# Optimization experiments

Measured on AMD Instinct MI355X. Metric: run time of the kernel, lower is better.

## Reference

```python
import jax, jax.numpy as jnp
import numpy as np

D = 512      # d_model
H = 8        # n_head
NL = 3       # encoder layers
FF = 2048    # torch TransformerEncoderLayer default dim_feedforward
HID = 256    # hidden_size
ACT = 12     # action_size
NOBJ = 89    # num_objects
BAND = 17    # tril(diagonal=-17) -> keys older than 16 steps banned


def setup_inputs() -> dict:
    key = jax.random.key(0)
    ks = iter(jax.random.split(key, 48))
    rn = lambda shape, s=0.02: jax.random.normal(next(ks), shape, jnp.float32) * s
    b, seq = 16, 512
    inp = {
        'state_input': jax.random.normal(next(ks), (b, seq, 3, 16, 16), jnp.float32),
        'goal_input': jax.random.normal(next(ks), (b, seq, 300), jnp.float32),
        # encoders (stand-ins for obs_enc / lang_enc)
        'W_obs': rn((256, 3 * 16 * 16)), 'b_obs': rn((256,)),
        'W_lang': rn((256, 300)), 'b_lang': rn((256,)),
        # input projection 512 -> 512
        'W_in': rn((D, 512)), 'b_in': rn((D,)),
        # per-layer transformer params, stacked on layer dim
        'Wqkv': rn((NL, 3 * D, D)), 'bqkv': rn((NL, 3 * D)),
        'Wo': rn((NL, D, D)), 'bo': rn((NL, D)),
        'W1': rn((NL, FF, D)), 'b1': rn((NL, FF)),
        'W2': rn((NL, D, FF)), 'b2': rn((NL, D)),
        'g1': jnp.ones((NL, D)), 'bt1': jnp.zeros((NL, D)),
        'g2': jnp.ones((NL, D)), 'bt2': jnp.zeros((NL, D)),
        # output heads
        'W_outp': rn((HID, D)), 'b_outp': rn((HID,)),
        'W_a1': rn((ACT, HID)), 'b_a1': rn((ACT,)),
        'W_a2': rn((NOBJ, HID)), 'b_a2': rn((NOBJ,)),
    }
    return inp


def _ln(y, g, bt):
    m = y.mean(-1, keepdims=True)
    v = y.var(-1, keepdims=True)
    return (y - m) / jnp.sqrt(v + 1e-5) * g + bt


def _encoder(x, mask_add, Wqkv, bqkv, Wo, bo, W1, b1, W2, b2, g1, bt1, g2, bt2):
    b, n, _ = x.shape
    dh = D // H
    scale = 1.0 / np.sqrt(dh)
    for l in range(NL):
        qkv = x @ Wqkv[l].T + bqkv[l]
        q, k, v = jnp.split(qkv, 3, axis=-1)
        hd = lambda t: t.reshape(b, n, H, dh).transpose(0, 2, 1, 3)  # [b,h,n,dh]
        q, k, v = hd(q), hd(k), hd(v)
        sc = jnp.einsum('bhqd,bhkd->bhqk', q, k) * scale + mask_add
        a = jax.nn.softmax(sc, axis=-1)
        o = jnp.einsum('bhqk,bhkd->bhqd', a, v).transpose(0, 2, 1, 3).reshape(b, n, D)
        o = o @ Wo[l].T + bo[l]
        x = _ln(x + o, g1[l], bt1[l])             # post-LN (torch default)
        f = jax.nn.relu(x @ W1[l].T + b1[l]) @ W2[l].T + b2[l]
        x = _ln(x + f, g2[l], bt2[l])
    return x


def reference(state_input, goal_input, W_obs, b_obs, W_lang, b_lang, W_in, b_in,
              Wqkv, bqkv, Wo, bo, W1, b1, W2, b2, g1, bt1, g2, bt2,
              W_outp, b_outp, W_a1, b_a1, W_a2, b_a2):
    b, s = state_input.shape[:2]
    st = state_input.reshape(b, s, -1) @ W_obs.T + b_obs          # obs_enc
    lg = goal_input @ W_lang.T + b_lang                            # lang_enc
    x = jnp.concatenate([st, lg], axis=-1) @ W_in.T + b_in        # [b,s,D]
    # key padding mask; sentinel token appended (causal_mask=False branch)
    pad = ~jnp.any(goal_input != -1, axis=-1)                      # [b,s]
    pad = jnp.concatenate([pad, jnp.zeros((b, 1), bool)], axis=1)
    x = jnp.concatenate([x, jnp.zeros((b, 1, D), x.dtype)], axis=1)
    n = s + 1
    i = jnp.arange(n)
    # banned: tril(-17) | triu(1)  -> attend only to keys in [i-16, i]
    mask2 = ((i[:, None] - i[None, :]) >= BAND) | (i[None, :] > i[:, None])
    banned = mask2[None, None, :, :] | pad[:, None, None, :]
    mask_add = jnp.where(banned, jnp.float32(-1e9), jnp.float32(0.0))
    x = _encoder(x, mask_add, Wqkv, bqkv, Wo, bo, W1, b1, W2, b2, g1, bt1, g2, bt2)
    out = x[:, :-1, :]                                             # drop sentinel
    h = out @ W_outp.T + b_outp
    l1 = h @ W_a1.T + b_a1
    l2 = h @ W_a2.T + b_a2
    return jnp.concatenate([l1, l2], axis=-1)                      # [b,s,101]
```

## Files before the change

kernel.cpp:

```cpp
#include <hip/hip_runtime.h>

#define D 512
#define H 8
#define NL 3
#define FFD 2048
#define HID 256
#define BAND 17
#define BATCH 16
#define SEQ 512
#define MTOK (BATCH * SEQ)
#define NOUT 101
#define NOUTP 128

typedef unsigned short u16;
typedef __attribute__((ext_vector_type(8))) short short8;
typedef __attribute__((ext_vector_type(4))) float f32x4;
typedef __attribute__((ext_vector_type(8))) unsigned short u16x8;

__device__ inline float bf2f(u16 u) {
    union { unsigned int i; float f; } x; x.i = ((unsigned int)u) << 16; return x.f;
}
__device__ inline u16 f2bf(float f) {
    union { float f; unsigned int i; } x; x.f = f;
    unsigned int r = x.i + 0x7fffu + ((x.i >> 16) & 1u);
    return (u16)(r >> 16);
}

__device__ __forceinline__ void gload_lds16(const u16* g, u16* l) {
    __builtin_amdgcn_global_load_lds(
        (const __attribute__((address_space(1))) unsigned int*)(g),
        (__attribute__((address_space(3))) unsigned int*)(l),
        16, 0, 0);
}

#define BM 128
#define BN 128
#define BK 32

__global__ __launch_bounds__(512) void gemm_kernel(
    const u16* __restrict__ A, int lda,
    const u16* __restrict__ B, int ldb,
    const float* __restrict__ bias,
    float* __restrict__ Cf, int ldcf,
    u16* __restrict__ Cb0, u16* __restrict__ Cb1, int ldcb,
    int M, int N, int K, int relu)
{
    __shared__ u16 As[3][BM * BK];
    __shared__ u16 Bs[3][BN * BK];
    const int tid  = threadIdx.x;
    const int lane = tid & 63;
    const int wv   = tid >> 6;
    const int wr = wv >> 2, wc = wv & 3;

    const int nb  = gridDim.x * gridDim.y;
    const int bid = blockIdx.y * gridDim.x + blockIdx.x;
    const int tile = (bid & 7) * (nb >> 3) + (bid >> 3);
    const int m0 = (tile / gridDim.x) * BM;
    const int n0 = (tile % gridDim.x) * BN;
    const int kz = blockIdx.z * K;

    f32x4 acc[4][2] = {};

    const int srow = lane >> 2;
    const int schunk = (lane & 3) ^ ((srow >> 1) & 3);
    const size_t aoff = (size_t)(m0 + wv * 16 + srow) * lda + kz + schunk * 8;
    const size_t boff = (size_t)(n0 + wv * 16 + srow) * ldb + kz + schunk * 8;

    const int frow = lane & 15;
    const int q    = lane >> 4;
    const int rcol = ((q ^ ((frow >> 1) & 3)) << 3);

    #define STAGE(buf, k0)                                             \
        do {                                                           \
            gload_lds16(A + aoff + (k0), &As[buf][wv * 16 * BK]);      \
            gload_lds16(B + boff + (k0), &Bs[buf][wv * 16 * BK]);      \
        } while (0)

    #define COMPUTE(buf)                                                            \
        do {                                                                        \
            short8 af[4], bf[2];                                                    \
            _Pragma("unroll")                                                       \
            for (int i = 0; i < 4; ++i)                                             \
                af[i] = *(const short8*)&As[buf][(wr * 64 + i * 16 + frow) * BK + rcol]; \
            _Pragma("unroll")                                                       \
            for (int j = 0; j < 2; ++j)                                             \
                bf[j] = *(const short8*)&Bs[buf][(wc * 32 + j * 16 + frow) * BK + rcol]; \
            _Pragma("unroll")                                                       \
            for (int i = 0; i < 4; ++i)                                             \
                _Pragma("unroll")                                                   \
                for (int j = 0; j < 2; ++j)                                         \
                    acc[i][j] = __builtin_amdgcn_mfma_f32_16x16x32_bf16(            \
                        af[i], bf[j], acc[i][j], 0, 0, 0);                          \
        } while (0)

    const int nt = K >> 5;
    STAGE(0, 0);
    STAGE(1, 32);
    int cur = 0;
    for (int t = 0; t < nt - 2; ++t) {
        int s = cur + 2; if (s >= 3) s -= 3;
        STAGE(s, (t + 2) << 5);
        asm volatile("s_waitcnt vmcnt(4)" ::: "memory");
        __builtin_amdgcn_s_barrier();
        __builtin_amdgcn_sched_barrier(0);
        COMPUTE(cur);
        __builtin_amdgcn_s_barrier();
        ++cur; if (cur >= 3) cur = 0;
    }
    asm volatile("s_waitcnt vmcnt(2)" ::: "memory");
    __builtin_amdgcn_s_barrier();
    __builtin_amdgcn_sched_barrier(0);
    COMPUTE(cur);
    __builtin_amdgcn_s_barrier();
    ++cur; if (cur >= 3) cur = 0;
    asm volatile("s_waitcnt vmcnt(0)" ::: "memory");
    __builtin_amdgcn_s_barrier();
    __builtin_amdgcn_sched_barrier(0);
    COMPUTE(cur);

    #undef STAGE
    #undef COMPUTE

    u16* Cb = blockIdx.z ? Cb1 : Cb0;
    const bool addb = (bias != nullptr) && (blockIdx.z == 0);

    const int crow0 = (lane >> 4) * 4;
    const int ccol  = lane & 15;
    #pragma unroll
    for (int j = 0; j < 2; ++j) {
        int gcol = n0 + wc * 32 + j * 16 + ccol;
        if (gcol >= N) continue;
        float bv = addb ? bias[gcol] : 0.f;
        #pragma unroll
        for (int i = 0; i < 4; ++i) {
            #pragma unroll
            for (int r = 0; r < 4; ++r) {
                int grow = m0 + wr * 64 + i * 16 + crow0 + r;
                float v = acc[i][j][r] + bv;
                if (relu) v = fmaxf(v, 0.f);
                if (Cf) Cf[(size_t)grow * ldcf + gcol] = v;
                if (Cb) Cb[(size_t)grow * ldcb + gcol] = f2bf(v);
            }
        }
    }
}

#define CHUNK 128
#define KSLOT 144
#define VT_LD 152

__global__ __launch_bounds__(512) void attn_kernel(
    const u16* __restrict__ qkv, const unsigned char* __restrict__ pad,
    u16* __restrict__ o)
{
    __shared__ u16 Vt[64 * VT_LD];
    __shared__ u16 Pl[8 * 16 * 40];
    __shared__ unsigned char padl[KSLOT];

    const int tid = threadIdx.x, lane = tid & 63, wv = tid >> 6;
    const int b = blockIdx.z, h = blockIdx.y, c0 = blockIdx.x * CHUNK;
    const u16* base = qkv + (size_t)b * SEQ * (3 * D);

    for (int s = tid; s < KSLOT * 4; s += 512) {
        int t = s >> 2, dq = (s & 3) * 16;
        int j = c0 - 16 + t; if (j < 0) j = 0;
        const u16* vrow = base + (size_t)j * (3 * D) + 2 * D + h * 64 + dq;
        u16 tmp[16];
        *(u16x8*)&tmp[0] = *(const u16x8*)&vrow[0];
        *(u16x8*)&tmp[8] = *(const u16x8*)&vrow[8];
        #pragma unroll
        for (int d = 0; d < 16; ++d)
            Vt[(dq + d) * VT_LD + t] = tmp[d];
    }
    if (tid < KSLOT) {
        int j = c0 - 16 + tid;
        padl[tid] = (j >= 0) ? pad[b * SEQ + j] : (unsigned char)1;
    }
    __syncthreads();

    const int qi0 = wv * 16;
    const int i0  = c0 + qi0;
    const int frow = lane & 15;
    const int g    = lane >> 4;
    const int kg8  = g * 8;
    const int g4   = g * 4;

    short8 qf[2];
    #pragma unroll
    for (int kk = 0; kk < 2; ++kk)
        qf[kk] = *(const short8*)&base[(size_t)(i0 + frow) * (3 * D) + h * 64 + kk * 32 + kg8];

    f32x4 sacc[2] = {};
    #pragma unroll
    for (int jb = 0; jb < 2; ++jb) {
        int jrow = i0 - 16 + jb * 16 + frow; if (jrow < 0) jrow = 0;
        const u16* kbase = base + (size_t)jrow * (3 * D) + D + h * 64;
        #pragma unroll
        for (int kk = 0; kk < 2; ++kk) {
            short8 kf = *(const short8*)&kbase[kk * 32 + kg8];
            sacc[jb] = __builtin_amdgcn_mfma_f32_16x16x32_bf16(qf[kk], kf, sacc[jb], 0, 0, 0);
        }
    }

    float sv[2][4];
    #pragma unroll
    for (int jb = 0; jb < 2; ++jb) {
        int s = jb * 16 + frow;
        int jg = i0 - 16 + s;
        bool padk = (jg < 0) || padl[qi0 + s];
        #pragma unroll
        for (int r = 0; r < 4; ++r) {
            int qq = g4 + r;
            bool banned = (s < qq) || (s > qq + 16) || padk;
            sv[jb][r] = sacc[jb][r] * 0.125f + (banned ? -1e9f : 0.f);
        }
    }

    float ex[2][4], rdn[4];
    #pragma unroll
    for (int r = 0; r < 4; ++r) {
        float m = fmaxf(sv[0][r], sv[1][r]);
        #pragma unroll
        for (int off = 1; off < 16; off <<= 1) m = fmaxf(m, __shfl_xor(m, off));
        float e0 = __expf(sv[0][r] - m);
        float e1 = __expf(sv[1][r] - m);
        float dsum = e0 + e1;
        #pragma unroll
        for (int off = 1; off < 16; off <<= 1) dsum += __shfl_xor(dsum, off);
        ex[0][r] = e0; ex[1][r] = e1;
        rdn[r] = 1.f / dsum;
    }

    u16* Pw = &Pl[wv * 640];
    #pragma unroll
    for (int jb = 0; jb < 2; ++jb)
        #pragma unroll
        for (int r = 0; r < 4; ++r)
            Pw[(g4 + r) * 40 + jb * 16 + frow] = f2bf(ex[jb][r]);
    short8 pa = *(const short8*)&Pw[frow * 40 + kg8];

    f32x4 oacc[4] = {};
    #pragma unroll
    for (int nb = 0; nb < 4; ++nb) {
        short8 vf = *(const short8*)&Vt[(nb * 16 + frow) * VT_LD + qi0 + kg8];
        oacc[nb] = __builtin_amdgcn_mfma_f32_16x16x32_bf16(pa, vf, oacc[nb], 0, 0, 0);
    }

    #pragma unroll
    for (int r = 0; r < 4; ++r) {
        size_t row = (size_t)(b * SEQ + i0 + g4 + r);
        #pragma unroll
        for (int nb = 0; nb < 4; ++nb)
            o[row * D + h * 64 + nb * 16 + frow] = f2bf(oacc[nb][r] * rdn[r]);
    }
}

__global__ __launch_bounds__(256) void resln_kernel(
    const u16* __restrict__ xin,
    const u16* __restrict__ d0, const u16* __restrict__ d1,
    const float* __restrict__ g, const float* __restrict__ bt,
    u16* __restrict__ xb)
{
    int row  = blockIdx.x * 4 + (threadIdx.x >> 6);
    int lane = threadIdx.x & 63;
    u16x8 xv = *(const u16x8*)(xin + (size_t)row * D + lane * 8);
    u16x8 dv0 = *(const u16x8*)(d0 + (size_t)row * D + lane * 8);
    u16x8 dv1 = *(const u16x8*)(d1 + (size_t)row * D + lane * 8);

    float y[8];
    float s = 0.f, s2 = 0.f;
    #pragma unroll
    for (int c = 0; c < 8; ++c) {
        y[c] = bf2f(xv[c]) + bf2f(dv0[c]) + bf2f(dv1[c]);
        s += y[c]; s2 += y[c] * y[c];
    }
    #pragma unroll
    for (int off = 32; off > 0; off >>= 1) {
        s  += __shfl_xor(s, off);
        s2 += __shfl_xor(s2, off);
    }
    float mean = s * (1.f / D);
    float var  = s2 * (1.f / D) - mean * mean;
    float inv  = rsqrtf(fmaxf(var, 0.f) + 1e-5f);

    f32x4 gv0 = ((const f32x4*)g)[lane * 2],  gv1 = ((const f32x4*)g)[lane * 2 + 1];
    f32x4 bv0 = ((const f32x4*)bt)[lane * 2], bv1 = ((const f32x4*)bt)[lane * 2 + 1];
    u16x8 ob;
    #pragma unroll
    for (int c = 0; c < 4; ++c) {
        ob[c]     = f2bf((y[c] - mean) * inv * gv0[c] + bv0[c]);
        ob[c + 4] = f2bf((y[c + 4] - mean) * inv * gv1[c] + bv1[c]);
    }
    *(u16x8*)(xb + (size_t)row * D + lane * 8) = ob;
}

__global__ __launch_bounds__(256) void pad_kernel(
    const float* __restrict__ goal, unsigned char* __restrict__ pad)
{
    int row  = blockIdx.x * 4 + (threadIdx.x >> 6);
    int lane = threadIdx.x & 63;
    const f32x4* gr = (const f32x4*)(goal + (size_t)row * 300);
    bool any = false;
    for (int c4 = lane; c4 < 75; c4 += 64) {
        f32x4 v = gr[c4];
        any |= (v[0] != -1.f) | (v[1] != -1.f) | (v[2] != -1.f) | (v[3] != -1.f);
    }
    unsigned long long b = __ballot(any);
    if (lane == 0) pad[row] = (b == 0ull) ? 1 : 0;
}

struct CvtJob { const float* src; u16* dstb; float* dstf; int n; int mode; };
struct CvtArgs { CvtJob j[15]; int blk0[16]; };

__global__ __launch_bounds__(256) void cvt_kernel(CvtArgs a) {
    const int bx = blockIdx.x;
    int jid = 0;
    #pragma unroll 1
    while (jid < 14 && bx >= a.blk0[jid + 1]) ++jid;
    const CvtJob jb = a.j[jid];
    const int i0 = (bx - a.blk0[jid]) * 2048 + threadIdx.x * 8;
    if (i0 >= jb.n) return;

    if (jb.mode == 0) {
        if (i0 + 8 <= jb.n) {
            f32x4 v0 = *(const f32x4*)(jb.src + i0);
            f32x4 v1 = *(const f32x4*)(jb.src + i0 + 4);
            u16x8 o;
            #pragma unroll
            for (int c = 0; c < 4; ++c) { o[c] = f2bf(v0[c]); o[c + 4] = f2bf(v1[c]); }
            *(u16x8*)(jb.dstb + i0) = o;
        } else {
            for (int e = 0; e < 8 && i0 + e < jb.n; ++e) jb.dstb[i0 + e] = f2bf(jb.src[i0 + e]);
        }
    } else if (jb.mode == 2) {
        int r = (int)((unsigned)i0 / 320u);
        int c = i0 - r * 320;
        const float* s = jb.src + (size_t)r * 300 + c;
        u16x8 o;
        if (c + 8 <= 300) {
            f32x4 v0 = *(const f32x4*)s;
            f32x4 v1 = *(const f32x4*)(s + 4);
            #pragma unroll
            for (int cc = 0; cc < 4; ++cc) { o[cc] = f2bf(v0[cc]); o[cc + 4] = f2bf(v1[cc]); }
        } else {
            #pragma unroll
            for (int e = 0; e < 8; ++e) o[e] = (c + e < 300) ? f2bf(s[e]) : (u16)0;
        }
        *(u16x8*)(jb.dstb + i0) = o;
    } else if (jb.mode == 1) {
        for (int e = 0; e < 8 && i0 + e < jb.n; ++e) jb.dstf[i0 + e] = jb.src[i0 + e];
    } else {
        u16x8 z = {0, 0, 0, 0, 0, 0, 0, 0};
        *(u16x8*)(jb.dstb + i0) = z;
    }
}


extern "C" void kernel_launch(void* const* d_in, const int* in_sizes, int n_in,
                              void* d_out, int out_size, void* d_ws, size_t ws_size,
                              hipStream_t stream)
{
    const float* state  = (const float*)d_in[0];
    const float* goal   = (const float*)d_in[1];
    const float* W_obs  = (const float*)d_in[2];
    const float* b_obs  = (const float*)d_in[3];
    const float* W_lang = (const float*)d_in[4];
    const float* b_lang = (const float*)d_in[5];
    const float* W_in   = (const float*)d_in[6];
    const float* b_in   = (const float*)d_in[7];
    const float* Wqkv   = (const float*)d_in[8];
    const float* bqkv   = (const float*)d_in[9];
    const float* Wo     = (const float*)d_in[10];
    const float* bo     = (const float*)d_in[11];
    const float* W1     = (const float*)d_in[12];
    const float* b1     = (const float*)d_in[13];
    const float* W2     = (const float*)d_in[14];
    const float* b2     = (const float*)d_in[15];
    const float* g1     = (const float*)d_in[16];
    const float* bt1    = (const float*)d_in[17];
    const float* g2     = (const float*)d_in[18];
    const float* bt2    = (const float*)d_in[19];
    const float* W_outp = (const float*)d_in[20];
    const float* b_outp = (const float*)d_in[21];
    const float* W_a1   = (const float*)d_in[22];
    const float* b_a1   = (const float*)d_in[23];
    const float* W_a2   = (const float*)d_in[24];
    const float* b_a2   = (const float*)d_in[25];

    char* ws = (char*)d_ws;
    size_t off = 0;
    auto alloc = [&](size_t bytes) -> void* {
        void* p = ws + off;
        off = (off + bytes + 255) & ~(size_t)255;
        return p;
    };

    u16* wqkv_b  = (u16*)alloc((size_t)NL * 1536 * D * 2);
    u16* wo_b    = (u16*)alloc((size_t)NL * D * D * 2);
    u16* w1_b    = (u16*)alloc((size_t)NL * FFD * D * 2);
    u16* w2_b    = (u16*)alloc((size_t)NL * D * FFD * 2);
    u16* wobs_b  = (u16*)alloc((size_t)256 * 768 * 2);
    u16* wlang_b = (u16*)alloc((size_t)256 * 320 * 2);
    u16* win_b   = (u16*)alloc((size_t)D * D * 2);
    u16* woutp_b = (u16*)alloc((size_t)HID * D * 2);
    u16* wa_b    = (u16*)alloc((size_t)NOUTP * HID * 2);
    float* ba_f  = (float*)alloc((size_t)NOUT * 4);
    u16* state_b = (u16*)alloc((size_t)MTOK * 768 * 2);
    u16* goal_b  = (u16*)alloc((size_t)MTOK * 320 * 2);
    u16* feat_b  = (u16*)alloc((size_t)MTOK * D * 2);
    u16* x_b     = (u16*)alloc((size_t)MTOK * D * 2);
    u16* qkv_b   = (u16*)alloc((size_t)MTOK * 3 * D * 2);
    u16* o_b     = (u16*)alloc((size_t)MTOK * D * 2);
    u16* delta_b = (u16*)alloc((size_t)MTOK * D * 2);
    u16* h1_b    = (u16*)alloc((size_t)MTOK * FFD * 2);
    u16* hout_b  = (u16*)alloc((size_t)MTOK * HID * 2);
    unsigned char* pad_u8 = (unsigned char*)alloc(MTOK);
    u16* delta2_b = state_b;
    (void)ws_size; (void)in_sizes; (void)n_in; (void)out_size;

    CvtArgs ca;
    int nj = 0, blks = 0;
    auto addj = [&](const float* s, u16* db, float* df, int n, int mode) {
        ca.j[nj].src = s; ca.j[nj].dstb = db; ca.j[nj].dstf = df;
        ca.j[nj].n = n; ca.j[nj].mode = mode;
        ca.blk0[nj] = blks;
        blks += (n + 2047) / 2048;
        ++nj;
    };
    addj(state,  state_b, nullptr, MTOK * 768, 0);
    addj(goal,   goal_b,  nullptr, MTOK * 320, 2);
    addj(Wqkv,   wqkv_b,  nullptr, NL * 1536 * D, 0);
    addj(Wo,     wo_b,    nullptr, NL * D * D, 0);
    addj(W1,     w1_b,    nullptr, NL * FFD * D, 0);
    addj(W2,     w2_b,    nullptr, NL * D * FFD, 0);
    addj(W_obs,  wobs_b,  nullptr, 256 * 768, 0);
    addj(W_lang, wlang_b, nullptr, 256 * 320, 2);
    addj(W_in,   win_b,   nullptr, D * D, 0);
    addj(W_outp, woutp_b, nullptr, HID * D, 0);
    addj(W_a1,   wa_b,            nullptr, 12 * HID, 0);
    addj(W_a2,   wa_b + 12 * HID, nullptr, 89 * HID, 0);
    addj(nullptr, wa_b + NOUT * HID, nullptr, (NOUTP - NOUT) * HID, 3);
    addj(b_a1,   nullptr, ba_f,      12, 1);
    addj(b_a2,   nullptr, ba_f + 12, 89, 1);
    ca.blk0[nj] = blks;
    cvt_kernel<<<blks, 256, 0, stream>>>(ca);

    pad_kernel<<<MTOK / 4, 256, 0, stream>>>(goal, pad_u8);

    auto gemm = [&](const u16* A, int lda, const u16* B, int ldb, const float* bias,
                    float* Cf, int ldcf, u16* Cb0, u16* Cb1, int ldcb,
                    int N, int K, int relu, int ksplit) {
        dim3 grid((N + BN - 1) / BN, MTOK / BM, ksplit);
        gemm_kernel<<<grid, 512, 0, stream>>>(A, lda, B, ldb, bias, Cf, ldcf,
                                              Cb0, Cb1, ldcb, MTOK, N, K / ksplit, relu);
    };

    gemm(state_b, 768, wobs_b, 768, b_obs, nullptr, 0, feat_b, nullptr, D, 256, 768, 0, 1);
    gemm(goal_b, 320, wlang_b, 320, b_lang, nullptr, 0, feat_b + 256, nullptr, D, 256, 320, 0, 1);
    gemm(feat_b, D, win_b, D, b_in, nullptr, 0, x_b, nullptr, D, D, D, 0, 1);

    for (int l = 0; l < NL; ++l) {
        gemm(x_b, D, wqkv_b + (size_t)l * 1536 * D, D, bqkv + l * 1536,
             nullptr, 0, qkv_b, nullptr, 3 * D, 3 * D, D, 0, 1);
        {
            dim3 grid(SEQ / CHUNK, H, BATCH);
            attn_kernel<<<grid, 512, 0, stream>>>(qkv_b, pad_u8, o_b);
        }
        gemm(o_b, D, wo_b + (size_t)l * D * D, D, bo + l * D,
             nullptr, 0, delta_b, delta2_b, D, D, D, 0, 2);
        resln_kernel<<<MTOK / 4, 256, 0, stream>>>(x_b, delta_b, delta2_b,
                                                   g1 + l * D, bt1 + l * D, x_b);
        gemm(x_b, D, w1_b + (size_t)l * FFD * D, D, b1 + l * FFD,
             nullptr, 0, h1_b, nullptr, FFD, FFD, D, 1, 1);
        gemm(h1_b, FFD, w2_b + (size_t)l * D * FFD, FFD, b2 + l * D,
             nullptr, 0, delta_b, delta2_b, D, D, FFD, 0, 2);
        resln_kernel<<<MTOK / 4, 256, 0, stream>>>(x_b, delta_b, delta2_b,
                                                   g2 + l * D, bt2 + l * D, x_b);
    }

    gemm(x_b, D, woutp_b, D, b_outp, nullptr, 0, hout_b, nullptr, HID, HID, D, 0, 1);
    gemm(hout_b, HID, wa_b, HID, ba_f, (float*)d_out, NOUT, nullptr, nullptr, 0, NOUT, HID, 0, 1);
}
```

Before: 402.5 us.

## Double K-tile depth to 64 and switch GEMM to two-stage LDS pipeline

Raises the GEMM K-tile from 32 to 64 and replaces the three-buffer LDS pipeline with a double buffer. Each wave now issues four async global-to-LDS loads per stage, and the XOR swizzle is widened to 8 chunks so fragment reads avoid bank conflicts. The goal is to halve the number of barriers and loop iterations per K. In exchange, prefetch depth drops from two tiles ahead to one, which can expose more load latency.

```diff
diff --git a/kernel.cpp b/kernel.cpp
--- a/kernel.cpp
+++ b/kernel.cpp
@@ -35,7 +35,7 @@
 
 #define BM 128
 #define BN 128
-#define BK 32
+#define BK 64
 
 __global__ __launch_bounds__(512) void gemm_kernel(
     const u16* __restrict__ A, int lda,
@@ -45,8 +45,8 @@
     u16* __restrict__ Cb0, u16* __restrict__ Cb1, int ldcb,
     int M, int N, int K, int relu)
 {
-    __shared__ u16 As[3][BM * BK];
-    __shared__ u16 Bs[3][BN * BK];
+    __shared__ u16 As[2][BM * BK];
+    __shared__ u16 Bs[2][BN * BK];
     const int tid  = threadIdx.x;
     const int lane = tid & 63;
     const int wv   = tid >> 6;
@@ -61,58 +61,63 @@
 
     f32x4 acc[4][2] = {};
 
-    const int srow = lane >> 2;
-    const int schunk = (lane & 3) ^ ((srow >> 1) & 3);
-    const size_t aoff = (size_t)(m0 + wv * 16 + srow) * lda + kz + schunk * 8;
-    const size_t boff = (size_t)(n0 + wv * 16 + srow) * ldb + kz + schunk * 8;
+    const int srow8 = lane >> 3;
+    const int schunk = (lane & 7) ^ srow8;
+    const size_t aoff0 = (size_t)(m0 + wv * 16 + srow8) * lda + kz + schunk * 8;
+    const size_t aoff1 = aoff0 + 8 * lda;
+    const size_t boff0 = (size_t)(n0 + wv * 16 + srow8) * ldb + kz + schunk * 8;
+    const size_t boff1 = boff0 + 8 * ldb;
 
     const int frow = lane & 15;
     const int q    = lane >> 4;
-    const int rcol = ((q ^ ((frow >> 1) & 3)) << 3);
-
-    #define STAGE(buf, k0)                                             \
-        do {                                                           \
-            gload_lds16(A + aoff + (k0), &As[buf][wv * 16 * BK]);      \
-            gload_lds16(B + boff + (k0), &Bs[buf][wv * 16 * BK]);      \
+    const int rc0 = ((q ^ (frow & 7)) << 3);
+    const int rc1 = (((4 + q) ^ (frow & 7)) << 3);
+
+    #define STAGE(buf, k0)                                                    \
+        do {                                                                  \
+            gload_lds16(A + aoff0 + (k0), &As[buf][(wv * 16 + 0) * BK]);      \
+            gload_lds16(A + aoff1 + (k0), &As[buf][(wv * 16 + 8) * BK]);      \
+            gload_lds16(B + boff0 + (k0), &Bs[buf][(wv * 16 + 0) * BK]);      \
+            gload_lds16(B + boff1 + (k0), &Bs[buf][(wv * 16 + 8) * BK]);      \
         } while (0)
 
     #define COMPUTE(buf)                                                            \
         do {                                                                        \
-            short8 af[4], bf[2];                                                    \
+            short8 af[4][2], bf[2][2];                                              \
             _Pragma("unroll")                                                       \
-            for (int i = 0; i < 4; ++i)                                             \
-                af[i] = *(const short8*)&As[buf][(wr * 64 + i * 16 + frow) * BK + rcol]; \
+            for (int i = 0; i < 4; ++i) {                                           \
+                const u16* rp = &As[buf][(wr * 64 + i * 16 + frow) * BK];           \
+                af[i][0] = *(const short8*)&rp[rc0];                                \
+                af[i][1] = *(const short8*)&rp[rc1];                                \
+            }                                                                       \
             _Pragma("unroll")                                                       \
-            for (int j = 0; j < 2; ++j)                                             \
-                bf[j] = *(const short8*)&Bs[buf][(wc * 32 + j * 16 + frow) * BK + rcol]; \
+            for (int j = 0; j < 2; ++j) {                                           \
+                const u16* rp = &Bs[buf][(wc * 32 + j * 16 + frow) * BK];           \
+                bf[j][0] = *(const short8*)&rp[rc0];                                \
+                bf[j][1] = *(const short8*)&rp[rc1];                                \
+            }                                                                       \
             _Pragma("unroll")                                                       \
-            for (int i = 0; i < 4; ++i)                                             \
+            for (int kk = 0; kk < 2; ++kk)                                          \
                 _Pragma("unroll")                                                   \
-                for (int j = 0; j < 2; ++j)                                         \
-                    acc[i][j] = __builtin_amdgcn_mfma_f32_16x16x32_bf16(            \
-                        af[i], bf[j], acc[i][j], 0, 0, 0);                          \
+                for (int i = 0; i < 4; ++i)                                         \
+                    _Pragma("unroll")                                               \
+                    for (int j = 0; j < 2; ++j)                                     \
+                        acc[i][j] = __builtin_amdgcn_mfma_f32_16x16x32_bf16(        \
+                            af[i][kk], bf[j][kk], acc[i][j], 0, 0, 0);              \
         } while (0)
 
-    const int nt = K >> 5;
+    const int nt = K >> 6;
     STAGE(0, 0);
-    STAGE(1, 32);
     int cur = 0;
-    for (int t = 0; t < nt - 2; ++t) {
-        int s = cur + 2; if (s >= 3) s -= 3;
-        STAGE(s, (t + 2) << 5);
+    for (int t = 0; t < nt - 1; ++t) {
+        STAGE(cur ^ 1, (t + 1) << 6);
         asm volatile("s_waitcnt vmcnt(4)" ::: "memory");
         __builtin_amdgcn_s_barrier();
         __builtin_amdgcn_sched_barrier(0);
         COMPUTE(cur);
         __builtin_amdgcn_s_barrier();
-        ++cur; if (cur >= 3) cur = 0;
-    }
-    asm volatile("s_waitcnt vmcnt(2)" ::: "memory");
-    __builtin_amdgcn_s_barrier();
-    __builtin_amdgcn_sched_barrier(0);
-    COMPUTE(cur);
-    __builtin_amdgcn_s_barrier();
-    ++cur; if (cur >= 3) cur = 0;
+        cur ^= 1;
+    }
     asm volatile("s_waitcnt vmcnt(0)" ::: "memory");
     __builtin_amdgcn_s_barrier();
     __builtin_amdgcn_sched_barrier(0);
```

After: 369.4 us, median of 2. 8.2% less time.
